# Kernel tuning notes

Measured on AMD Instinct MI355X. Metric: run time of the kernel, lower is better.

Reference implementation:

```python
import jax, jax.numpy as jnp
import numpy as np

NUM_EXPERTS = 8
TOP_K = 2
D_IN = 1024
D_OUT = 1024
N_TOKENS = 8192


def setup_inputs() -> dict:
    key = jax.random.key(0)
    ks = jax.random.split(key, 7)
    s_in = 1.0 / np.sqrt(D_IN)
    s_out = 1.0 / np.sqrt(D_OUT)
    return {
        "x": jax.random.normal(ks[0], (N_TOKENS, D_IN), dtype=jnp.float32),
        # stacked expert params: fc1 [E, D_in, D_out], fc2 [E, D_out, D_out]
        "W1": jax.random.uniform(ks[1], (NUM_EXPERTS, D_IN, D_OUT), jnp.float32, -s_in, s_in),
        "b1": jax.random.uniform(ks[2], (NUM_EXPERTS, D_OUT), jnp.float32, -s_in, s_in),
        "W2": jax.random.uniform(ks[3], (NUM_EXPERTS, D_OUT, D_OUT), jnp.float32, -s_out, s_out),
        "b2": jax.random.uniform(ks[4], (NUM_EXPERTS, D_OUT), jnp.float32, -s_out, s_out),
        "Wg": jax.random.uniform(ks[5], (D_IN, NUM_EXPERTS), jnp.float32, -s_in, s_in),
        "bg": jax.random.uniform(ks[6], (NUM_EXPERTS,), jnp.float32, -s_in, s_in),
    }


def reference(x, W1, b1, W2, b2, Wg, bg):
    n = x.shape[0]
    # gating
    gate_logits = x @ Wg + bg                      # [N, E]
    gate_weights = jax.nn.softmax(gate_logits, axis=1)
    if TOP_K < NUM_EXPERTS:
        topk_vals, topk_idx = jax.lax.top_k(gate_weights, TOP_K)  # [N, K]
        rows = jnp.arange(n)[:, None]
        gate_weights = jnp.zeros_like(gate_weights).at[rows, topk_idx].set(topk_vals)
    # dense all-expert MLP fan-out (faithful to the original wasteful compute)
    h = jax.nn.relu(jnp.einsum('nd,edh->enh', x, W1) + b1[:, None, :])  # [E, N, H]
    y = jnp.einsum('enh,eho->eno', h, W2) + b2[:, None, :]               # [E, N, O]
    # weighted combine over experts
    out = jnp.einsum('ne,eno->no', gate_weights, y)                      # [N, O]
    return out
```

## Files before the change

kernel.cpp:

```cpp
#include <hip/hip_runtime.h>

#define NUM_E 8
#define N_TOK 8192
#define DIM 1024

typedef __attribute__((ext_vector_type(8))) short short8;
typedef __attribute__((ext_vector_type(4))) float f32x4;

__device__ __forceinline__ unsigned short f2bf(float f) {
  unsigned int u = __float_as_uint(f);
  u = (u + 0x7fffu + ((u >> 16) & 1u)) >> 16;
  return (unsigned short)u;
}

__device__ __forceinline__ void async16(const unsigned short* g, unsigned short* l) {
  __builtin_amdgcn_global_load_lds((const __attribute__((address_space(1))) void*)g,
                                   (__attribute__((address_space(3))) void*)l,
                                   16, 0, 0);
}

__global__ __launch_bounds__(256) void prep_gate_kernel(
    const float* __restrict__ x, const float* __restrict__ Wg,
    const float* __restrict__ bg, int* __restrict__ tok_top,
    float2* __restrict__ tok_wts, unsigned short* __restrict__ xb,
    float* __restrict__ out) {
  {
    float4* oz = (float4*)(out + (size_t)blockIdx.x * 4096);
    const float4 z4 = {0.f, 0.f, 0.f, 0.f};
#pragma unroll
    for (int i = 0; i < 4; ++i) oz[i * 256 + threadIdx.x] = z4;
  }
  const int wave = threadIdx.x >> 6;
  const int lane = threadIdx.x & 63;
  const int n = blockIdx.x * 4 + wave;
  const float4* xr = (const float4*)(x + (size_t)n * DIM);
  unsigned short* xbr = xb + (size_t)n * DIM;
  float acc[NUM_E];
#pragma unroll
  for (int e = 0; e < NUM_E; ++e) acc[e] = 0.f;
#pragma unroll
  for (int it = 0; it < 4; ++it) {
    float4 xv = xr[it * 64 + lane];
    const float4* wr = (const float4*)Wg + (size_t)(it * 256 + lane * 4) * 2;
    float xs[4] = {xv.x, xv.y, xv.z, xv.w};
    union { unsigned short u[4]; uint2 v; } oo;
    oo.u[0] = f2bf(xv.x); oo.u[1] = f2bf(xv.y);
    oo.u[2] = f2bf(xv.z); oo.u[3] = f2bf(xv.w);
    *(uint2*)(xbr + it * 256 + lane * 4) = oo.v;
#pragma unroll
    for (int dd = 0; dd < 4; ++dd) {
      float4 wa = wr[dd * 2 + 0];
      float4 wb = wr[dd * 2 + 1];
      acc[0] += xs[dd] * wa.x; acc[1] += xs[dd] * wa.y;
      acc[2] += xs[dd] * wa.z; acc[3] += xs[dd] * wa.w;
      acc[4] += xs[dd] * wb.x; acc[5] += xs[dd] * wb.y;
      acc[6] += xs[dd] * wb.z; acc[7] += xs[dd] * wb.w;
    }
  }
#pragma unroll
  for (int e = 0; e < NUM_E; ++e)
#pragma unroll
    for (int off = 32; off > 0; off >>= 1)
      acc[e] += __shfl_down(acc[e], off);
  if (lane == 0) {
    float p[NUM_E];
    float mx = -1e30f;
#pragma unroll
    for (int e = 0; e < NUM_E; ++e) { p[e] = acc[e] + bg[e]; mx = fmaxf(mx, p[e]); }
    float ss = 0.f;
#pragma unroll
    for (int e = 0; e < NUM_E; ++e) { p[e] = expf(p[e] - mx); ss += p[e]; }
    float inv = 1.f / ss;
    int i0 = 0;
#pragma unroll
    for (int e = 1; e < NUM_E; ++e) if (p[e] > p[i0]) i0 = e;
    int i1 = (i0 == 0) ? 1 : 0;
#pragma unroll
    for (int e = 0; e < NUM_E; ++e) if (e != i0 && p[e] > p[i1]) i1 = e;
    tok_top[n] = i0 | (i1 << 8);
    tok_wts[n] = make_float2(p[i0] * inv, p[i1] * inv);
  }
}

__global__ __launch_bounds__(256) void prep_w_gate2_kernel(
    const float* __restrict__ W1, const float* __restrict__ W2,
    unsigned short* __restrict__ W1T, unsigned short* __restrict__ W2T,
    const int* __restrict__ tok_top, const float2* __restrict__ tok_wts,
    int* __restrict__ counts, int* __restrict__ tok_idx,
    float* __restrict__ tok_w) {
  __shared__ float s[64][65];
  __shared__ int wsum[4];
  __shared__ int btot;
  if (blockIdx.x < 4096) {
    const int bx  = blockIdx.x;
    const int mat = bx >> 8;
    const int tk  = (bx >> 4) & 15;
    const int tn  = bx & 15;
    const float* src;
    unsigned short* dst;
    if (mat < 8) { src = W1 + (size_t)mat * (DIM * DIM); dst = W1T + (size_t)mat * (DIM * DIM); }
    else         { src = W2 + (size_t)(mat - 8) * (DIM * DIM); dst = W2T + (size_t)(mat - 8) * (DIM * DIM); }
    const int k0 = tk * 64, n0 = tn * 64;
    const int t = threadIdx.x;
    {
      const int rr = t >> 4;
      const int c4 = (t & 15) * 4;
#pragma unroll
      for (int i = 0; i < 4; ++i) {
        const int k = i * 16 + rr;
        float4 v = *(const float4*)&src[(size_t)(k0 + k) * DIM + n0 + c4];
        s[c4 + 0][k] = v.x; s[c4 + 1][k] = v.y;
        s[c4 + 2][k] = v.z; s[c4 + 3][k] = v.w;
      }
    }
    __syncthreads();
    {
      const int kq = (t & 7) * 8;
      const int nn = t >> 3;
#pragma unroll
      for (int r = 0; r < 2; ++r) {
        const int n = r * 32 + nn;
        union { unsigned short us[8]; uint4 v; } o;
#pragma unroll
        for (int j = 0; j < 8; ++j) o.us[j] = f2bf(s[n][kq + j]);
        *(uint4*)(dst + (size_t)(n0 + n) * DIM + k0 + kq) = o.v;
      }
    }
  } else {
    const int e = blockIdx.x - 4096;
    const int t = threadIdx.x;
    const int lane = t & 63;
    const int wave = t >> 6;
    unsigned mask = 0;
    int cnt = 0;
#pragma unroll 8
    for (int j = 0; j < 32; ++j) {
      int top = tok_top[t * 32 + j];
      bool m = ((top & 0xff) == e) || (((top >> 8) & 0xff) == e);
      mask |= (unsigned)m << j;
      cnt += m;
    }
    int inc = cnt;
#pragma unroll
    for (int off = 1; off < 64; off <<= 1) {
      int v = __shfl_up(inc, off);
      if (lane >= off) inc += v;
    }
    if (lane == 63) wsum[wave] = inc;
    __syncthreads();
    if (t < 4) {
      int v = wsum[t];
      int ssum = v;
#pragma unroll
      for (int off = 1; off < 4; off <<= 1) {
        int u = __shfl_up(ssum, off);
        if (lane >= off) ssum += u;
      }
      wsum[t] = ssum - v;
      if (t == 3) btot = ssum;
    }
    __syncthreads();
    int slot = wsum[wave] + inc - cnt;
#pragma unroll 8
    for (int j = 0; j < 32; ++j) {
      if ((mask >> j) & 1u) {
        int n = t * 32 + j;
        int top = tok_top[n];
        float2 ww = tok_wts[n];
        bool m0 = (top & 0xff) == e;
        tok_idx[e * N_TOK + slot] = n;
        tok_w[e * N_TOK + slot] = m0 ? ww.x : ww.y;
        slot++;
      }
    }
    if (t == 0) counts[e] = btot;
  }
}


template <bool FC1>
__global__ __launch_bounds__(256, 4) void moe_gemm_kernel(
    const unsigned short* __restrict__ A_src,
    const unsigned short* __restrict__ wT,
    const float* __restrict__ bias,
    const int* __restrict__ counts,
    const int* __restrict__ tok_idx,
    const float* __restrict__ tok_w,
    unsigned short* __restrict__ h_out,
    float* __restrict__ out)
{
  const int bid = blockIdx.x;
  const int xcd = bid & 7;
  const int mt  = xcd * 17 + (bid >> 6);
  const int nt  = (bid >> 3) & 7;

  int e = -1, m0 = 0, base = 0;
  {
    int acc_tiles = 0, acc_rows = 0;
#pragma unroll
    for (int i = 0; i < NUM_E; ++i) {
      int c = counts[i];
      int t = (c + 127) >> 7;
      if (mt >= acc_tiles && mt < acc_tiles + t) {
        e = i; m0 = (mt - acc_tiles) * 128; base = acc_rows;
      }
      acc_tiles += t;
      acc_rows += t * 128;
    }
  }
  if (e < 0) return;
  const int count = counts[e];
  const int n0 = nt * 128;

  const int tid  = threadIdx.x;
  const int wave = tid >> 6;
  const int lane = tid & 63;
  const int l15  = lane & 15;
  const int quad = lane >> 4;
  const int wm   = wave & 1;
  const int wn   = wave >> 1;

  __shared__ unsigned short sA[2 * 4096];
  __shared__ unsigned short sB[2 * 4096];
  __shared__ int   s_tok[128];
  __shared__ float s_w[128];

  if (!FC1 && tid < 128) {
    int slot = m0 + tid;
    int cs = slot < count ? slot : count - 1;
    s_tok[tid] = tok_idx[e * N_TOK + cs];
    s_w[tid]   = slot < count ? tok_w[e * N_TOK + slot] : 0.f;
  }

  const int r0 = 32 * wave + l15;
  const int r1 = r0 + 16;
  size_t aOff0, aOff1;
  if (FC1) {
    int s0 = m0 + r0; s0 = s0 < count ? s0 : count - 1;
    int s1 = m0 + r1; s1 = s1 < count ? s1 : count - 1;
    aOff0 = (size_t)tok_idx[e * N_TOK + s0] * DIM;
    aOff1 = (size_t)tok_idx[e * N_TOK + s1] * DIM;
  } else {
    aOff0 = (size_t)(base + m0 + r0) * DIM;
    aOff1 = (size_t)(base + m0 + r1) * DIM;
  }
  const unsigned short* wte = wT + (size_t)e * DIM * DIM;
  const size_t bOff0 = (size_t)(n0 + r0) * DIM;
  const size_t bOff1 = (size_t)(n0 + r1) * DIM;
  const int kl = quad * 8;
  const int c0 = (2 * wave + 0) * 512;
  const int c1 = (2 * wave + 1) * 512;

  const f32x4 vzero = {0.f, 0.f, 0.f, 0.f};
  f32x4 acc[4][4];
#pragma unroll
  for (int i = 0; i < 4; ++i)
#pragma unroll
    for (int j = 0; j < 4; ++j) acc[i][j] = vzero;

  for (int k0 = 0; k0 < DIM; k0 += 64) {
    async16(A_src + aOff0 + k0 + kl,      &sA[c0]);
    async16(A_src + aOff1 + k0 + kl,      &sA[c1]);
    async16(A_src + aOff0 + k0 + 32 + kl, &sA[4096 + c0]);
    async16(A_src + aOff1 + k0 + 32 + kl, &sA[4096 + c1]);
    async16(wte + bOff0 + k0 + kl,        &sB[c0]);
    async16(wte + bOff1 + k0 + kl,        &sB[c1]);
    async16(wte + bOff0 + k0 + 32 + kl,   &sB[4096 + c0]);
    async16(wte + bOff1 + k0 + 32 + kl,   &sB[4096 + c1]);
    __syncthreads();
#pragma unroll
    for (int s = 0; s < 2; ++s) {
      short8 af[4], bfr[4];
#pragma unroll
      for (int i = 0; i < 4; ++i)
        af[i] = *(const short8*)&sA[s * 4096 + (wm * 4 + i) * 512 + lane * 8];
#pragma unroll
      for (int j = 0; j < 4; ++j)
        bfr[j] = *(const short8*)&sB[s * 4096 + (wn * 4 + j) * 512 + lane * 8];
#pragma unroll
      for (int i = 0; i < 4; ++i)
#pragma unroll
        for (int j = 0; j < 4; ++j)
          acc[i][j] = __builtin_amdgcn_mfma_f32_16x16x32_bf16(af[i], bfr[j], acc[i][j], 0, 0, 0);
    }
    __syncthreads();
  }

  float bv[4];
#pragma unroll
  for (int j = 0; j < 4; ++j)
    bv[j] = bias[e * DIM + n0 + (wn * 4 + j) * 16 + l15];

  if (FC1) {
#pragma unroll
    for (int i = 0; i < 4; ++i) {
      const int rbase = (wm * 4 + i) * 16 + quad * 4;
#pragma unroll
      for (int r = 0; r < 4; ++r) {
        const int slot = m0 + rbase + r;
        if (slot < count) {
          unsigned short* hp = h_out + (size_t)(base + slot) * DIM + n0;
#pragma unroll
          for (int j = 0; j < 4; ++j) {
            float v = acc[i][j][r] + bv[j];
            v = v > 0.f ? v : 0.f;
            hp[(wn * 4 + j) * 16 + l15] = f2bf(v);
          }
        }
      }
    }
  } else {
#pragma unroll
    for (int i = 0; i < 4; ++i) {
      const int rbase = (wm * 4 + i) * 16 + quad * 4;
#pragma unroll
      for (int r = 0; r < 4; ++r) {
        const int slot = m0 + rbase + r;
        if (slot < count) {
          const int rl = rbase + r;
          const int tok = s_tok[rl];
          const float w = s_w[rl];
          float* op = out + (size_t)tok * DIM + n0;
#pragma unroll
          for (int j = 0; j < 4; ++j) {
            float v = acc[i][j][r] + bv[j];
            atomicAdd(&op[(wn * 4 + j) * 16 + l15], w * v);
          }
        }
      }
    }
  }
}


extern "C" void kernel_launch(void* const* d_in, const int* in_sizes, int n_in,
                              void* d_out, int out_size, void* d_ws, size_t ws_size,
                              hipStream_t stream) {
  const float* x  = (const float*)d_in[0];
  const float* W1 = (const float*)d_in[1];
  const float* b1 = (const float*)d_in[2];
  const float* W2 = (const float*)d_in[3];
  const float* b2 = (const float*)d_in[4];
  const float* Wg = (const float*)d_in[5];
  const float* bg = (const float*)d_in[6];
  float* out = (float*)d_out;

  char* ws = (char*)d_ws;
  int*            counts  = (int*)(ws);
  int*            tok_idx = (int*)(ws + 1024);
  float*          tok_w   = (float*)(ws + 263168);
  unsigned short* xb      = (unsigned short*)(ws + 525312);
  unsigned short* w1t     = (unsigned short*)(ws + 525312 + 16777216ull);
  unsigned short* w2t     = (unsigned short*)(ws + 525312 + 2ull * 16777216ull);
  unsigned short* hb      = (unsigned short*)(ws + 525312 + 3ull * 16777216ull);
  size_t gate_off = 525312 + 3ull * 16777216ull + 35651584ull;
  int*            tok_top = (int*)(ws + gate_off);
  float2*         tok_wts = (float2*)(ws + gate_off + 32768);

  prep_gate_kernel<<<2048, 256, 0, stream>>>(x, Wg, bg, tok_top, tok_wts, xb, out);
  prep_w_gate2_kernel<<<4104, 256, 0, stream>>>(W1, W2, w1t, w2t,
                                                tok_top, tok_wts, counts, tok_idx, tok_w);
  moe_gemm_kernel<true><<<1088, 256, 0, stream>>>(
      xb, w1t, b1, counts, tok_idx, tok_w, hb, nullptr);
  moe_gemm_kernel<false><<<1088, 256, 0, stream>>>(
      hb, w2t, b2, counts, tok_idx, tok_w, nullptr, out);
}
```

Before: 378.9 us.

## Overlap weight transposes with gating and FC1, shrink FC2 tiles

```diff
diff --git a/kernel.cpp b/kernel.cpp
--- a/kernel.cpp
+++ b/kernel.cpp
@@ -19,20 +19,61 @@
                                    16, 0, 0);
 }
 
-__global__ __launch_bounds__(256) void prep_gate_kernel(
+__device__ __forceinline__ void wtile_transpose(const float* src, unsigned short* dst,
+                                                int tk, int tn, float (*s)[65]) {
+  const int k0 = tk * 64, n0 = tn * 64;
+  const int t = threadIdx.x;
+  {
+    const int rr = t >> 4;
+    const int c4 = (t & 15) * 4;
+#pragma unroll
+    for (int i = 0; i < 4; ++i) {
+      const int k = i * 16 + rr;
+      float4 v = *(const float4*)&src[(size_t)(k0 + k) * DIM + n0 + c4];
+      s[c4 + 0][k] = v.x; s[c4 + 1][k] = v.y;
+      s[c4 + 2][k] = v.z; s[c4 + 3][k] = v.w;
+    }
+  }
+  __syncthreads();
+  {
+    const int kq = (t & 7) * 8;
+    const int nn = t >> 3;
+#pragma unroll
+    for (int r = 0; r < 2; ++r) {
+      const int n = r * 32 + nn;
+      union { unsigned short us[8]; uint4 v; } o;
+#pragma unroll
+      for (int j = 0; j < 8; ++j) o.us[j] = f2bf(s[n][kq + j]);
+      *(uint4*)(dst + (size_t)(n0 + n) * DIM + k0 + kq) = o.v;
+    }
+  }
+}
+
+__global__ __launch_bounds__(256) void prep_gate_w1_kernel(
     const float* __restrict__ x, const float* __restrict__ Wg,
     const float* __restrict__ bg, int* __restrict__ tok_top,
     float2* __restrict__ tok_wts, unsigned short* __restrict__ xb,
-    float* __restrict__ out) {
+    float* __restrict__ out,
+    const float* __restrict__ W1, unsigned short* __restrict__ W1T) {
+  __shared__ float s[64][65];
+  const int bid = blockIdx.x;
+  if (bid & 1) {
+    const int wv = bid >> 1;
+    wtile_transpose(W1 + (size_t)(wv >> 8) * (DIM * DIM),
+                    W1T + (size_t)(wv >> 8) * (DIM * DIM),
+                    (wv >> 4) & 15, wv & 15, s);
+    return;
+  }
+  const int gb = bid >> 1;
   {
-    float4* oz = (float4*)(out + (size_t)blockIdx.x * 4096);
+    float4* oz = (float4*)(out + (size_t)gb * 4096);
     const float4 z4 = {0.f, 0.f, 0.f, 0.f};
 #pragma unroll
     for (int i = 0; i < 4; ++i) oz[i * 256 + threadIdx.x] = z4;
   }
   const int wave = threadIdx.x >> 6;
   const int lane = threadIdx.x & 63;
-  const int n = blockIdx.x * 4 + wave;
+  const int n = gb * 4 + wave;
   const float4* xr = (const float4*)(x + (size_t)n * DIM);
   unsigned short* xbr = xb + (size_t)n * DIM;
   float acc[NUM_E];
@@ -82,117 +123,86 @@
   }
 }
 
-__global__ __launch_bounds__(256) void prep_w_gate2_kernel(
-    const float* __restrict__ W1, const float* __restrict__ W2,
-    unsigned short* __restrict__ W1T, unsigned short* __restrict__ W2T,
-    const int* __restrict__ tok_top, const float2* __restrict__ tok_wts,
-    int* __restrict__ counts, int* __restrict__ tok_idx,
-    float* __restrict__ tok_w) {
-  __shared__ float s[64][65];
+__global__ __launch_bounds__(256) void gate2_kernel(const int* __restrict__ tok_top,
+                                                    const float2* __restrict__ tok_wts,
+                                                    int* __restrict__ counts,
+                                                    int* __restrict__ tok_idx,
+                                                    float* __restrict__ tok_w) {
   __shared__ int wsum[4];
   __shared__ int btot;
-  if (blockIdx.x < 4096) {
-    const int bx  = blockIdx.x;
-    const int mat = bx >> 8;
-    const int tk  = (bx >> 4) & 15;
-    const int tn  = bx & 15;
-    const float* src;
-    unsigned short* dst;
-    if (mat < 8) { src = W1 + (size_t)mat * (DIM * DIM); dst = W1T + (size_t)mat * (DIM * DIM); }
-    else         { src = W2 + (size_t)(mat - 8) * (DIM * DIM); dst = W2T + (size_t)(mat - 8) * (DIM * DIM); }
-    const int k0 = tk * 64, n0 = tn * 64;
-    const int t = threadIdx.x;
-    {
-      const int rr = t >> 4;
-      const int c4 = (t & 15) * 4;
-#pragma unroll
-      for (int i = 0; i < 4; ++i) {
-        const int k = i * 16 + rr;
-        float4 v = *(const float4*)&src[(size_t)(k0 + k) * DIM + n0 + c4];
-        s[c4 + 0][k] = v.x; s[c4 + 1][k] = v.y;
-        s[c4 + 2][k] = v.z; s[c4 + 3][k] = v.w;
-      }
-    }
-    __syncthreads();
-    {
-      const int kq = (t & 7) * 8;
-      const int nn = t >> 3;
-#pragma unroll
-      for (int r = 0; r < 2; ++r) {
-        const int n = r * 32 + nn;
-        union { unsigned short us[8]; uint4 v; } o;
-#pragma unroll
-        for (int j = 0; j < 8; ++j) o.us[j] = f2bf(s[n][kq + j]);
-        *(uint4*)(dst + (size_t)(n0 + n) * DIM + k0 + kq) = o.v;
-      }
-    }
-  } else {
-    const int e = blockIdx.x - 4096;
-    const int t = threadIdx.x;
-    const int lane = t & 63;
-    const int wave = t >> 6;
-    unsigned mask = 0;
-    int cnt = 0;
+  const int e = blockIdx.x;
+  const int t = threadIdx.x;
+  const int lane = t & 63;
+  const int wave = t >> 6;
+  unsigned mask = 0;
+  int cnt = 0;
 #pragma unroll 8
-    for (int j = 0; j < 32; ++j) {
-      int top = tok_top[t * 32 + j];
-      bool m = ((top & 0xff) == e) || (((top >> 8) & 0xff) == e);
-      mask |= (unsigned)m << j;
-      cnt += m;
-    }
-    int inc = cnt;
-#pragma unroll
-    for (int off = 1; off < 64; off <<= 1) {
-      int v = __shfl_up(inc, off);
-      if (lane >= off) inc += v;
-    }
-    if (lane == 63) wsum[wave] = inc;
-    __syncthreads();
-    if (t < 4) {
-      int v = wsum[t];
-      int ssum = v;
-#pragma unroll
-      for (int off = 1; off < 4; off <<= 1) {
-        int u = __shfl_up(ssum, off);
-        if (lane >= off) ssum += u;
-      }
-      wsum[t] = ssum - v;
-      if (t == 3) btot = ssum;
-    }
-    __syncthreads();
-    int slot = wsum[wave] + inc - cnt;
+  for (int j = 0; j < 32; ++j) {
+    int top = tok_top[t * 32 + j];
+    bool m = ((top & 0xff) == e) || (((top >> 8) & 0xff) == e);
+    mask |= (unsigned)m << j;
+    cnt += m;
+  }
+  int inc = cnt;
+#pragma unroll
+  for (int off = 1; off < 64; off <<= 1) {
+    int v = __shfl_up(inc, off);
+    if (lane >= off) inc += v;
+  }
+  if (lane == 63) wsum[wave] = inc;
+  __syncthreads();
+  if (t < 4) {
+    int v = wsum[t];
+    int ssum = v;
+#pragma unroll
+    for (int off = 1; off < 4; off <<= 1) {
+      int u = __shfl_up(ssum, off);
+      if (lane >= off) ssum += u;
+    }
+    wsum[t] = ssum - v;
+    if (t == 3) btot = ssum;
+  }
+  __syncthreads();
+  int slot = wsum[wave] + inc - cnt;
 #pragma unroll 8
-    for (int j = 0; j < 32; ++j) {
-      if ((mask >> j) & 1u) {
-        int n = t * 32 + j;
-        int top = tok_top[n];
-        float2 ww = tok_wts[n];
-        bool m0 = (top & 0xff) == e;
-        tok_idx[e * N_TOK + slot] = n;
-        tok_w[e * N_TOK + slot] = m0 ? ww.x : ww.y;
-        slot++;
-      }
-    }
-    if (t == 0) counts[e] = btot;
-  }
-}
-
-
-template <bool FC1>
-__global__ __launch_bounds__(256, 4) void moe_gemm_kernel(
+  for (int j = 0; j < 32; ++j) {
+    if ((mask >> j) & 1u) {
+      int n = t * 32 + j;
+      int top = tok_top[n];
+      float2 ww = tok_wts[n];
+      bool m0 = (top & 0xff) == e;
+      tok_idx[e * N_TOK + slot] = n;
+      tok_w[e * N_TOK + slot] = m0 ? ww.x : ww.y;
+      slot++;
+    }
+  }
+  if (t == 0) counts[e] = btot;
+}
+
+__global__ __launch_bounds__(256, 4) void fc1_w2t_kernel(
     const unsigned short* __restrict__ A_src,
     const unsigned short* __restrict__ wT,
+    const float* __restrict__ W2, unsigned short* __restrict__ W2T,
     const float* __restrict__ bias,
     const int* __restrict__ counts,
     const int* __restrict__ tok_idx,
-    const float* __restrict__ tok_w,
-    unsigned short* __restrict__ h_out,
-    float* __restrict__ out)
+    unsigned short* __restrict__ h_out)
 {
+  __shared__ __align__(16) unsigned char smem[33792];
   const int bid = blockIdx.x;
-  const int xcd = bid & 7;
-  const int mt  = xcd * 17 + (bid >> 6);
-  const int nt  = (bid >> 3) & 7;
+  const int role = bid % 3;
+  if (role != 0) {
+    const int wv = (bid / 3) * 2 + role - 1;
+    if (wv < 2048)
+      wtile_transpose(W2 + (size_t)(wv >> 8) * (DIM * DIM),
+                      W2T + (size_t)(wv >> 8) * (DIM * DIM),
+                      (wv >> 4) & 15, wv & 15, (float(*)[65])smem);
+    return;
+  }
+  const int xcd  = bid & 7;
+  const int rank = bid / 24;
+  const int mt   = xcd * 17 + (rank >> 3);
+  const int nt   = rank & 7;
 
   int e = -1, m0 = 0, base = 0;
   {
@@ -220,30 +230,15 @@
   const int wm   = wave & 1;
   const int wn   = wave >> 1;
 
-  __shared__ unsigned short sA[2 * 4096];
-  __shared__ unsigned short sB[2 * 4096];
-  __shared__ int   s_tok[128];
-  __shared__ float s_w[128];
-
-  if (!FC1 && tid < 128) {
-    int slot = m0 + tid;
-    int cs = slot < count ? slot : count - 1;
-    s_tok[tid] = tok_idx[e * N_TOK + cs];
-    s_w[tid]   = slot < count ? tok_w[e * N_TOK + slot] : 0.f;
-  }
+  unsigned short* sA = (unsigned short*)smem;
+  unsigned short* sB = (unsigned short*)(smem + 16384);
 
   const int r0 = 32 * wave + l15;
   const int r1 = r0 + 16;
-  size_t aOff0, aOff1;
-  if (FC1) {
-    int s0 = m0 + r0; s0 = s0 < count ? s0 : count - 1;
-    int s1 = m0 + r1; s1 = s1 < count ? s1 : count - 1;
-    aOff0 = (size_t)tok_idx[e * N_TOK + s0] * DIM;
-    aOff1 = (size_t)tok_idx[e * N_TOK + s1] * DIM;
-  } else {
-    aOff0 = (size_t)(base + m0 + r0) * DIM;
-    aOff1 = (size_t)(base + m0 + r1) * DIM;
-  }
+  int s0 = m0 + r0; s0 = s0 < count ? s0 : count - 1;
+  int s1 = m0 + r1; s1 = s1 < count ? s1 : count - 1;
+  const size_t aOff0 = (size_t)tok_idx[e * N_TOK + s0] * DIM;
+  const size_t aOff1 = (size_t)tok_idx[e * N_TOK + s1] * DIM;
   const unsigned short* wte = wT + (size_t)e * DIM * DIM;
   const size_t bOff0 = (size_t)(n0 + r0) * DIM;
   const size_t bOff1 = (size_t)(n0 + r1) * DIM;
@@ -291,41 +286,126 @@
   for (int j = 0; j < 4; ++j)
     bv[j] = bias[e * DIM + n0 + (wn * 4 + j) * 16 + l15];
 
-  if (FC1) {
-#pragma unroll
-    for (int i = 0; i < 4; ++i) {
-      const int rbase = (wm * 4 + i) * 16 + quad * 4;
-#pragma unroll
-      for (int r = 0; r < 4; ++r) {
-        const int slot = m0 + rbase + r;
-        if (slot < count) {
-          unsigned short* hp = h_out + (size_t)(base + slot) * DIM + n0;
-#pragma unroll
-          for (int j = 0; j < 4; ++j) {
-            float v = acc[i][j][r] + bv[j];
-            v = v > 0.f ? v : 0.f;
-            hp[(wn * 4 + j) * 16 + l15] = f2bf(v);
-          }
+#pragma unroll
+  for (int i = 0; i < 4; ++i) {
+    const int rbase = (wm * 4 + i) * 16 + quad * 4;
+#pragma unroll
+    for (int r = 0; r < 4; ++r) {
+      const int slot = m0 + rbase + r;
+      if (slot < count) {
+        unsigned short* hp = h_out + (size_t)(base + slot) * DIM + n0;
+#pragma unroll
+        for (int j = 0; j < 4; ++j) {
+          float v = acc[i][j][r] + bv[j];
+          v = v > 0.f ? v : 0.f;
+          hp[(wn * 4 + j) * 16 + l15] = f2bf(v);
         }
       }
     }
-  } else {
-#pragma unroll
-    for (int i = 0; i < 4; ++i) {
-      const int rbase = (wm * 4 + i) * 16 + quad * 4;
-#pragma unroll
-      for (int r = 0; r < 4; ++r) {
-        const int slot = m0 + rbase + r;
-        if (slot < count) {
-          const int rl = rbase + r;
-          const int tok = s_tok[rl];
-          const float w = s_w[rl];
-          float* op = out + (size_t)tok * DIM + n0;
-#pragma unroll
-          for (int j = 0; j < 4; ++j) {
-            float v = acc[i][j][r] + bv[j];
-            atomicAdd(&op[(wn * 4 + j) * 16 + l15], w * v);
-          }
+  }
+}
+
+__global__ __launch_bounds__(256) void fc2_kernel(
+    const unsigned short* __restrict__ A_src,
+    const unsigned short* __restrict__ wT,
+    const float* __restrict__ bias,
+    const int* __restrict__ counts,
+    const int* __restrict__ tok_idx,
+    const float* __restrict__ tok_w,
+    float* __restrict__ out)
+{
+  const int bid = blockIdx.x;
+  const int xcd = bid & 7;
+  const int mt  = xcd * 33 + (bid >> 6);
+  const int nt  = (bid >> 3) & 7;
+
+  int e = -1, m0 = 0, base = 0;
+  {
+    int at = 0, ar = 0;
+#pragma unroll
+    for (int i = 0; i < NUM_E; ++i) {
+      int c = counts[i];
+      int t = (c + 63) >> 6;
+      if (mt >= at && mt < at + t) { e = i; m0 = (mt - at) * 64; base = ar; }
+      at += t;
+      ar += ((c + 127) >> 7) * 128;
+    }
+  }
+  if (e < 0) return;
+  const int count = counts[e];
+  const int n0 = nt * 128;
+
+  const int tid  = threadIdx.x;
+  const int wave = tid >> 6;
+  const int lane = tid & 63;
+  const int l15  = lane & 15;
+  const int quad = lane >> 4;
+  const int wm   = wave & 1;
+  const int wn   = wave >> 1;
+
+  __shared__ unsigned short sA[4096];
+  __shared__ unsigned short sB[8192];
+
+  const size_t aOff  = (size_t)(base + m0 + 16 * wave + l15) * DIM + quad * 8;
+  const unsigned short* wte = wT + (size_t)e * DIM * DIM;
+  const size_t bOff0 = (size_t)(n0 + 32 * wave + l15) * DIM + quad * 8;
+  const size_t bOff1 = bOff0 + 16 * DIM;
+  const int cA  = wave * 512;
+  const int cB0 = 2 * wave * 512;
+  const int cB1 = cB0 + 512;
+
+  const f32x4 vzero = {0.f, 0.f, 0.f, 0.f};
+  f32x4 acc[2][4];
+#pragma unroll
+  for (int i = 0; i < 2; ++i)
+#pragma unroll
+    for (int j = 0; j < 4; ++j) acc[i][j] = vzero;
+
+  for (int k0 = 0; k0 < DIM; k0 += 64) {
+    async16(A_src + aOff + k0,       &sA[cA]);
+    async16(A_src + aOff + k0 + 32,  &sA[2048 + cA]);
+    async16(wte + bOff0 + k0,        &sB[cB0]);
+    async16(wte + bOff1 + k0,        &sB[cB1]);
+    async16(wte + bOff0 + k0 + 32,   &sB[4096 + cB0]);
+    async16(wte + bOff1 + k0 + 32,   &sB[4096 + cB1]);
+    __syncthreads();
+#pragma unroll
+    for (int s = 0; s < 2; ++s) {
+      short8 af[2], bfr[4];
+#pragma unroll
+      for (int i = 0; i < 2; ++i)
+        af[i] = *(const short8*)&sA[s * 2048 + (wm * 2 + i) * 512 + lane * 8];
+#pragma unroll
+      for (int j = 0; j < 4; ++j)
+        bfr[j] = *(const short8*)&sB[s * 4096 + (wn * 4 + j) * 512 + lane * 8];
+#pragma unroll
+      for (int i = 0; i < 2; ++i)
+#pragma unroll
+        for (int j = 0; j < 4; ++j)
+          acc[i][j] = __builtin_amdgcn_mfma_f32_16x16x32_bf16(af[i], bfr[j], acc[i][j], 0, 0, 0);
+    }
+    __syncthreads();
+  }
+
+  float bv[4];
+#pragma unroll
+  for (int j = 0; j < 4; ++j)
+    bv[j] = bias[e * DIM + n0 + (wn * 4 + j) * 16 + l15];
+
+#pragma unroll
+  for (int i = 0; i < 2; ++i) {
+    const int rbase = (wm * 2 + i) * 16 + quad * 4;
+#pragma unroll
+    for (int r = 0; r < 4; ++r) {
+      const int slot = m0 + rbase + r;
+      if (slot < count) {
+        const int tok = tok_idx[e * N_TOK + slot];
+        const float wgt = tok_w[e * N_TOK + slot];
+        float* op = out + (size_t)tok * DIM + n0;
+#pragma unroll
+        for (int j = 0; j < 4; ++j) {
+          float v = acc[i][j][r] + bv[j];
+          atomicAdd(&op[(wn * 4 + j) * 16 + l15], wgt * v);
         }
       }
     }
@@ -357,11 +437,10 @@
   int*            tok_top = (int*)(ws + gate_off);
   float2*         tok_wts = (float2*)(ws + gate_off + 32768);
 
-  prep_gate_kernel<<<2048, 256, 0, stream>>>(x, Wg, bg, tok_top, tok_wts, xb, out);
-  prep_w_gate2_kernel<<<4104, 256, 0, stream>>>(W1, W2, w1t, w2t,
-                                                tok_top, tok_wts, counts, tok_idx, tok_w);
-  moe_gemm_kernel<true><<<1088, 256, 0, stream>>>(
-      xb, w1t, b1, counts, tok_idx, tok_w, hb, nullptr);
-  moe_gemm_kernel<false><<<1088, 256, 0, stream>>>(
-      hb, w2t, b2, counts, tok_idx, tok_w, nullptr, out);
-}
+  prep_gate_w1_kernel<<<4096, 256, 0, stream>>>(x, Wg, bg, tok_top, tok_wts, xb,
+                                                out, W1, w1t);
+  gate2_kernel<<<8, 256, 0, stream>>>(tok_top, tok_wts, counts, tok_idx, tok_w);
+  fc1_w2t_kernel<<<3264, 256, 0, stream>>>(xb, w1t, W2, w2t, b1,
+                                           counts, tok_idx, hb);
+  fc2_kernel<<<2112, 256, 0, stream>>>(hb, w2t, b2, counts, tok_idx, tok_w, out);
+}
```

Result: slower. 419.7 us (+10.8%).
